# Kernel tuning notes

Measured on AMD Instinct MI355X. Metric: run time of the kernel, lower is better.

The kernel has to match this reference:

```python
import jax, jax.numpy as jnp
import numpy as np

NGRID, NLAYER = 8192, 24
NPERIODS, NOBS, NC = 50, 4096, 200
SIGMA = 1.0
VREF = 3.0          # reference crustal Vs (km/s) for depth-sensitivity scale
RAYLEIGH_FACTOR = 0.92


def setup_inputs() -> dict:
    key = jax.random.key(0)
    k1, k2, k3 = jax.random.split(key, 3)
    # S-wave velocity model, 2.0-4.0 km/s, flattened as in log_prob(Vs_flat)
    Vs_flat = (2.0 + 2.0 * jax.random.uniform(k1, (NGRID, NLAYER))).reshape(-1).astype(jnp.float32)
    # Ray-path averaging matrix: nonnegative, rows sum to 1 (slowness average)
    A = jax.random.uniform(k2, (NOBS, NGRID), dtype=jnp.float32)
    A = A / A.sum(axis=1, keepdims=True)
    # Beamforming energy spectra per observation pair: (Nobs, Nperiods, Nc)
    energy = jax.random.uniform(k3, (NOBS, NPERIODS, NC), dtype=jnp.float32)
    # Monotone phase-velocity axis per observation: (Nobs, Nc)
    c_axis = jnp.zeros((NOBS, NC), jnp.float32) + jnp.linspace(1.5, 5.0, NC, dtype=jnp.float32)
    thick = jnp.full((NLAYER,), 2.0, jnp.float32)          # 2 km layers
    periods = jnp.linspace(1.0, 60.0, NPERIODS, dtype=jnp.float32)
    return {"Vs_flat": Vs_flat, "A": A, "energy": energy, "c_axis": c_axis,
            "thick": thick, "periods": periods}


def _dispersion_all_cells(Vs, thick, periods):
    # Differentiable surrogate for the batched surf96 forward across all grid cells.
    # Vs: (G, L), thick: (L,), periods: (P,)  ->  c_true: (G, P)
    z = jnp.cumsum(thick) - 0.5 * thick                      # layer-center depths (L,)
    depth_scale = VREF * periods / 3.0                       # ~ sensing depth per period (P,)
    w = jnp.exp(-z[None, :] / depth_scale[:, None]) * thick[None, :]  # (P, L)
    w = w / w.sum(axis=1, keepdims=True)
    return RAYLEIGH_FACTOR * jnp.einsum('pl,gl->gp', w, Vs)  # (G, P)


def reference(Vs_flat, A, energy, c_axis, thick, periods):
    Vs = Vs_flat.reshape(NGRID, NLAYER)
    c_true = _dispersion_all_cells(Vs, thick, periods)       # (Ngrid, Nperiods)
    # _apply_A: slowness averaging along ray paths
    s_pred = A @ (1.0 / c_true)                              # (Nobs, Nperiods)
    c_pred = 1.0 / s_pred
    # _interp1d_torch, vectorized over all (obs, period) pairs
    idx = jax.vmap(jnp.searchsorted)(c_axis, c_pred)         # (Nobs, Nperiods)
    idx = jnp.clip(idx, 1, NC - 1)
    c0 = jnp.take_along_axis(c_axis, idx - 1, axis=1)
    c1 = jnp.take_along_axis(c_axis, idx, axis=1)
    e0 = jnp.take_along_axis(energy, (idx - 1)[:, :, None], axis=2)[..., 0]
    e1 = jnp.take_along_axis(energy, idx[:, :, None], axis=2)[..., 0]
    w = (c_pred - c0) / (c1 - c0 + 1e-12)
    e_interp = e0 + w * (e1 - e0)
    e_max = energy.max(axis=-1)                              # (Nobs, Nperiods)
    log_like = -jnp.sum(e_max - e_interp) / (SIGMA ** 2)
    return log_like
```

## Files before the change

### kernel.cpp

```cpp
#include <hip/hip_runtime.h>

#define NGRID 8192
#define NLAYER 24
#define NPERIODS 50
#define NOBS 4096
#define NC 200
#define PP 64
#define NSPLIT 16
#define GC (NGRID / NSPLIT)
#define KG 32
#define ASTR 36
#define NPW 13
#define NBINS 1024
#define OTILE 64
#define VREF 3.0f

__global__ __launch_bounds__(256) void k1_rpad(const float* __restrict__ Vs,
                                               const float* __restrict__ thick,
                                               const float* __restrict__ periods,
                                               float* __restrict__ r_pad,
                                               float* __restrict__ bins) {
    __shared__ float w_sh[NLAYER][NPERIODS];
    __shared__ float z_sh[NLAYER];
    int tid = threadIdx.x;
    if (blockIdx.x == 0) {
        for (int i = tid; i < NBINS; i += 256) bins[i] = 0.f;
    }
    if (tid < NLAYER) {
        float c = 0.f;
        for (int i = 0; i <= tid; ++i) c += thick[i];
        z_sh[tid] = c - 0.5f * thick[tid];
    }
    __syncthreads();
    if (tid < NPERIODS) {
        float ds = (VREF / 3.0f) * periods[tid];
        float tmp[NLAYER];
        float s = 0.f;
        #pragma unroll
        for (int l = 0; l < NLAYER; ++l) {
            float v = expf(-z_sh[l] / ds) * thick[l];
            tmp[l] = v; s += v;
        }
        float inv = 1.f / s;
        #pragma unroll
        for (int l = 0; l < NLAYER; ++l) w_sh[l][tid] = tmp[l] * inv;
    }
    __syncthreads();
    int idx = blockIdx.x * 256 + tid;
    int g = idx >> 6, p = idx & 63;
    float r = 0.f;
    if (p < NPERIODS) {
        const float4* vp = (const float4*)(Vs + (size_t)g * NLAYER);
        float s = 0.f;
        #pragma unroll
        for (int q = 0; q < NLAYER / 4; ++q) {
            float4 t = vp[q];
            s = fmaf(w_sh[4*q+0][p], t.x, s);
            s = fmaf(w_sh[4*q+1][p], t.y, s);
            s = fmaf(w_sh[4*q+2][p], t.z, s);
            s = fmaf(w_sh[4*q+3][p], t.w, s);
        }
        r = 1.0f / (0.92f * s);
    }
    r_pad[idx] = r;
}

__global__ __launch_bounds__(256) void k2_gemm(const float* __restrict__ A,
                                               const float* __restrict__ r_pad,
                                               float* __restrict__ partial_t) {
    __shared__ float Aw[OTILE * ASTR];
    int tid  = threadIdx.x;
    int lane = tid & 63;
    int wv   = __builtin_amdgcn_readfirstlane(tid >> 6);
    int o_base = blockIdx.x * OTILE;
    int split  = blockIdx.y;
    int pbase  = wv * NPW;

    float acc[NPW];
    #pragma unroll
    for (int p = 0; p < NPW; ++p) acc[p] = 0.f;

    int g_blk = split * GC;

    #pragma unroll 1
    for (int kt = 0; kt < GC / KG; ++kt) {
        int g0 = g_blk + kt * KG;
        __syncthreads();
        #pragma unroll
        for (int s = 0; s < 2; ++s) {
            int f   = s * 256 + tid;
            int row = f >> 3;
            int c4  = (f & 7) * 4;
            float4 t = *(const float4*)(A + (size_t)(o_base + row) * NGRID + g0 + c4);
            *(float4*)(Aw + row * ASTR + c4) = t;
        }
        __syncthreads();
        #pragma unroll 1
        for (int gg = 0; gg < KG; gg += 4) {
            float4 a4 = *(const float4*)(Aw + lane * ASTR + gg);
            const float* rr = r_pad + (size_t)(g0 + gg) * PP + pbase;
            #pragma unroll
            for (int j = 0; j < 4; ++j) {
                float aj = (j == 0) ? a4.x : (j == 1) ? a4.y : (j == 2) ? a4.z : a4.w;
                #pragma unroll
                for (int p = 0; p < NPW; ++p)
                    acc[p] = fmaf(aj, rr[j * PP + p], acc[p]);
            }
        }
    }

    float* outp = partial_t + (size_t)split * (NPERIODS * NOBS);
    #pragma unroll
    for (int p = 0; p < NPW; ++p) {
        int pp = pbase + p;
        if (pp < NPERIODS)
            outp[(size_t)pp * NOBS + o_base + lane] = acc[p];
    }
}

__global__ __launch_bounds__(256) void k2b_reduce(const float* __restrict__ partial_t,
                                                  float* __restrict__ cpred_t) {
    int idx = blockIdx.x * 256 + threadIdx.x;
    float s = 0.f;
    #pragma unroll
    for (int sp = 0; sp < NSPLIT; ++sp)
        s += partial_t[(size_t)sp * (NPERIODS * NOBS) + idx];
    cpred_t[idx] = 1.0f / s;
}

__global__ __launch_bounds__(256) void k3_main(const float* __restrict__ energy,
                                               const float* __restrict__ c_axis,
                                               const float* __restrict__ cpred_t,
                                               float* __restrict__ bins) {
    __shared__ float csh[NC];
    __shared__ float red[4];
    int tid  = threadIdx.x;
    int lane = tid & 63;
    int wv   = tid >> 6;
    int o    = blockIdx.x;

    if (tid < NC) csh[tid] = c_axis[(size_t)o * NC + tid];
    __syncthreads();

    bool act = lane < NC / 4;
    float4 ca = act ? *(const float4*)(csh + 4 * lane) : make_float4(9e30f, 9e30f, 9e30f, 9e30f);
    const float* ebase = energy + (size_t)o * NPERIODS * NC;
    float local = 0.f;

    for (int p0 = wv; p0 < NPERIODS; p0 += 8) {
        int p1 = p0 + 4;
        bool has1 = p1 < NPERIODS;
        int p1c = has1 ? p1 : p0;
        float cpA = cpred_t[(size_t)p0 * NOBS + o];
        float cpB = cpred_t[(size_t)p1c * NOBS + o];
        const float* erA = ebase + (size_t)p0 * NC;
        const float* erB = ebase + (size_t)p1c * NC;
        float4 eA = act ? *(const float4*)(erA + 4 * lane) : make_float4(-1e30f, -1e30f, -1e30f, -1e30f);
        float4 eB = act ? *(const float4*)(erB + 4 * lane) : make_float4(-1e30f, -1e30f, -1e30f, -1e30f);

        int cntA = __popcll(__ballot(ca.x < cpA)) + __popcll(__ballot(ca.y < cpA))
                 + __popcll(__ballot(ca.z < cpA)) + __popcll(__ballot(ca.w < cpA));
        int cntB = __popcll(__ballot(ca.x < cpB)) + __popcll(__ballot(ca.y < cpB))
                 + __popcll(__ballot(ca.z < cpB)) + __popcll(__ballot(ca.w < cpB));

        float mA = fmaxf(fmaxf(eA.x, eA.y), fmaxf(eA.z, eA.w));
        float mB = fmaxf(fmaxf(eB.x, eB.y), fmaxf(eB.z, eB.w));
        #pragma unroll
        for (int m = 32; m; m >>= 1) {
            mA = fmaxf(mA, __shfl_xor(mA, m, 64));
            mB = fmaxf(mB, __shfl_xor(mB, m, 64));
        }

        int iA = cntA < 1 ? 1 : (cntA > NC - 1 ? NC - 1 : cntA);
        int iB = cntB < 1 ? 1 : (cntB > NC - 1 ? NC - 1 : cntB);

        int a0 = iA - 1, a1 = iA, b0 = iB - 1, b1 = iB;
        float sA0 = ((a0 & 3) == 0) ? eA.x : ((a0 & 3) == 1) ? eA.y : ((a0 & 3) == 2) ? eA.z : eA.w;
        float sA1 = ((a1 & 3) == 0) ? eA.x : ((a1 & 3) == 1) ? eA.y : ((a1 & 3) == 2) ? eA.z : eA.w;
        float sB0 = ((b0 & 3) == 0) ? eB.x : ((b0 & 3) == 1) ? eB.y : ((b0 & 3) == 2) ? eB.z : eB.w;
        float sB1 = ((b1 & 3) == 0) ? eB.x : ((b1 & 3) == 1) ? eB.y : ((b1 & 3) == 2) ? eB.z : eB.w;
        float e0A = __shfl(sA0, a0 >> 2, 64), e1A = __shfl(sA1, a1 >> 2, 64);
        float e0B = __shfl(sB0, b0 >> 2, 64), e1B = __shfl(sB1, b1 >> 2, 64);

        float c0A = csh[a0], c1A = csh[a1];
        float c0B = csh[b0], c1B = csh[b1];
        float wA = (cpA - c0A) / (c1A - c0A + 1e-12f);
        float wB = (cpB - c0B) / (c1B - c0B + 1e-12f);
        float eiA = fmaf(wA, e1A - e0A, e0A);
        float eiB = fmaf(wB, e1B - e0B, e0B);
        local += mA - eiA;
        local += has1 ? (mB - eiB) : 0.f;
    }
    if (lane == 0) red[wv] = local;
    __syncthreads();
    if (tid == 0)
        atomicAdd(&bins[blockIdx.x & (NBINS - 1)], red[0] + red[1] + red[2] + red[3]);
}

__global__ __launch_bounds__(256) void k4_final(const float* __restrict__ bins,
                                                float* __restrict__ out) {
    __shared__ float red[4];
    int tid = threadIdx.x;
    float s = 0.f;
    for (int i = tid; i < NBINS; i += 256) s += bins[i];
    #pragma unroll
    for (int m = 32; m; m >>= 1) s += __shfl_xor(s, m, 64);
    int lane = tid & 63, wv = tid >> 6;
    if (lane == 0) red[wv] = s;
    __syncthreads();
    if (tid == 0) out[0] = -(red[0] + red[1] + red[2] + red[3]);
}

extern "C" void kernel_launch(void* const* d_in, const int* in_sizes, int n_in,
                              void* d_out, int out_size, void* d_ws, size_t ws_size,
                              hipStream_t stream) {
    const float* Vs      = (const float*)d_in[0];
    const float* A       = (const float*)d_in[1];
    const float* energy  = (const float*)d_in[2];
    const float* c_axis  = (const float*)d_in[3];
    const float* thick   = (const float*)d_in[4];
    const float* periods = (const float*)d_in[5];
    float* out = (float*)d_out;

    float* ws        = (float*)d_ws;
    float* r_pad     = ws;
    float* partial_t = r_pad + (size_t)NGRID * PP;
    float* cpred_t   = partial_t + (size_t)NSPLIT * NPERIODS * NOBS;
    float* bins      = cpred_t + (size_t)NPERIODS * NOBS;

    hipLaunchKernelGGL(k1_rpad, dim3((NGRID * 64) / 256), dim3(256), 0, stream,
                       Vs, thick, periods, r_pad, bins);
    hipLaunchKernelGGL(k2_gemm, dim3(NOBS / OTILE, NSPLIT), dim3(256), 0, stream,
                       A, r_pad, partial_t);
    hipLaunchKernelGGL(k2b_reduce, dim3((NPERIODS * NOBS) / 256), dim3(256), 0, stream,
                       partial_t, cpred_t);
    hipLaunchKernelGGL(k3_main, dim3(NOBS), dim3(256), 0, stream,
                       energy, c_axis, cpred_t, bins);
    hipLaunchKernelGGL(k4_final, dim3(1), dim3(256), 0, stream, bins, out);
}
```

Measured before the change: 391.2 us.

## Double-buffer A tiles in GEMM with 8 waves and stage energy in LDS

The GEMM kernel moves to 512 threads (8 waves, 7 periods each) and double-buffers the A tile in shared memory. The next tile's global load is issued before computing on the current one, and there is one barrier per iteration instead of two. The interpolation kernel now copies each observation's full energy block into padded shared memory and has lanes map to periods, with each wave scanning a quarter of the c axis for max and count. This replaces per-period ballots and shuffles. It raises LDS use to about 40KB per block in the interpolation kernel, which may limit occupancy.

```diff
diff --git a/kernel.cpp b/kernel.cpp
--- a/kernel.cpp
+++ b/kernel.cpp
@@ -9,8 +9,11 @@
 #define NSPLIT 16
 #define GC (NGRID / NSPLIT)
 #define KG 32
+#define NKT (GC / KG)
 #define ASTR 36
-#define NPW 13
+#define WPB 8
+#define NPW 7
+#define ESTR 201
 #define NBINS 1024
 #define OTILE 64
 #define VREF 3.0f
@@ -65,10 +68,10 @@
     r_pad[idx] = r;
 }
 
-__global__ __launch_bounds__(256) void k2_gemm(const float* __restrict__ A,
+__global__ __launch_bounds__(512) void k2_gemm(const float* __restrict__ A,
                                                const float* __restrict__ r_pad,
                                                float* __restrict__ partial_t) {
-    __shared__ float Aw[OTILE * ASTR];
+    __shared__ float Aw[2][OTILE * ASTR];
     int tid  = threadIdx.x;
     int lane = tid & 63;
     int wv   = __builtin_amdgcn_readfirstlane(tid >> 6);
@@ -81,23 +84,26 @@
     for (int p = 0; p < NPW; ++p) acc[p] = 0.f;
 
     int g_blk = split * GC;
+    int srow = tid >> 3;
+    int sc4  = (tid & 7) * 4;
+    const float* Abase = A + (size_t)(o_base + srow) * NGRID + sc4 + g_blk;
+
+    {
+        float4 t = *(const float4*)(Abase);
+        *(float4*)(&Aw[0][srow * ASTR + sc4]) = t;
+    }
 
     #pragma unroll 1
-    for (int kt = 0; kt < GC / KG; ++kt) {
+    for (int kt = 0; kt < NKT; ++kt) {
+        int cur = kt & 1;
+        __syncthreads();
+        int ktn = (kt + 1 < NKT) ? kt + 1 : NKT - 1;
+        float4 tnext = *(const float4*)(Abase + ktn * KG);
+
         int g0 = g_blk + kt * KG;
-        __syncthreads();
-        #pragma unroll
-        for (int s = 0; s < 2; ++s) {
-            int f   = s * 256 + tid;
-            int row = f >> 3;
-            int c4  = (f & 7) * 4;
-            float4 t = *(const float4*)(A + (size_t)(o_base + row) * NGRID + g0 + c4);
-            *(float4*)(Aw + row * ASTR + c4) = t;
-        }
-        __syncthreads();
         #pragma unroll 1
         for (int gg = 0; gg < KG; gg += 4) {
-            float4 a4 = *(const float4*)(Aw + lane * ASTR + gg);
+            float4 a4 = *(const float4*)(&Aw[cur][lane * ASTR + gg]);
             const float* rr = r_pad + (size_t)(g0 + gg) * PP + pbase;
             #pragma unroll
             for (int j = 0; j < 4; ++j) {
@@ -107,6 +113,7 @@
                     acc[p] = fmaf(aj, rr[j * PP + p], acc[p]);
             }
         }
+        *(float4*)(&Aw[cur ^ 1][srow * ASTR + sc4]) = tnext;
     }
 
     float* outp = partial_t + (size_t)split * (NPERIODS * NOBS);
@@ -132,69 +139,60 @@
                                                const float* __restrict__ c_axis,
                                                const float* __restrict__ cpred_t,
                                                float* __restrict__ bins) {
+    __shared__ float esh[NPERIODS * ESTR];
     __shared__ float csh[NC];
-    __shared__ float red[4];
+    __shared__ float cpsh[64];
+    __shared__ float cntp[4][64];
+    __shared__ float maxp[4][64];
     int tid  = threadIdx.x;
     int lane = tid & 63;
     int wv   = tid >> 6;
     int o    = blockIdx.x;
 
+    const float* eb = energy + (size_t)o * NPERIODS * NC;
+    for (int i = tid; i < (NPERIODS * NC) / 4; i += 256) {
+        int r_ = i / 50;
+        int c_ = (i - r_ * 50) * 4;
+        float4 v = *(const float4*)(eb + (size_t)i * 4);
+        float* d = esh + r_ * ESTR + c_;
+        d[0] = v.x; d[1] = v.y; d[2] = v.z; d[3] = v.w;
+    }
     if (tid < NC) csh[tid] = c_axis[(size_t)o * NC + tid];
-    __syncthreads();
-
-    bool act = lane < NC / 4;
-    float4 ca = act ? *(const float4*)(csh + 4 * lane) : make_float4(9e30f, 9e30f, 9e30f, 9e30f);
-    const float* ebase = energy + (size_t)o * NPERIODS * NC;
-    float local = 0.f;
-
-    for (int p0 = wv; p0 < NPERIODS; p0 += 8) {
-        int p1 = p0 + 4;
-        bool has1 = p1 < NPERIODS;
-        int p1c = has1 ? p1 : p0;
-        float cpA = cpred_t[(size_t)p0 * NOBS + o];
-        float cpB = cpred_t[(size_t)p1c * NOBS + o];
-        const float* erA = ebase + (size_t)p0 * NC;
-        const float* erB = ebase + (size_t)p1c * NC;
-        float4 eA = act ? *(const float4*)(erA + 4 * lane) : make_float4(-1e30f, -1e30f, -1e30f, -1e30f);
-        float4 eB = act ? *(const float4*)(erB + 4 * lane) : make_float4(-1e30f, -1e30f, -1e30f, -1e30f);
-
-        int cntA = __popcll(__ballot(ca.x < cpA)) + __popcll(__ballot(ca.y < cpA))
-                 + __popcll(__ballot(ca.z < cpA)) + __popcll(__ballot(ca.w < cpA));
-        int cntB = __popcll(__ballot(ca.x < cpB)) + __popcll(__ballot(ca.y < cpB))
-                 + __popcll(__ballot(ca.z < cpB)) + __popcll(__ballot(ca.w < cpB));
-
-        float mA = fmaxf(fmaxf(eA.x, eA.y), fmaxf(eA.z, eA.w));
-        float mB = fmaxf(fmaxf(eB.x, eB.y), fmaxf(eB.z, eB.w));
-        #pragma unroll
-        for (int m = 32; m; m >>= 1) {
-            mA = fmaxf(mA, __shfl_xor(mA, m, 64));
-            mB = fmaxf(mB, __shfl_xor(mB, m, 64));
-        }
-
-        int iA = cntA < 1 ? 1 : (cntA > NC - 1 ? NC - 1 : cntA);
-        int iB = cntB < 1 ? 1 : (cntB > NC - 1 ? NC - 1 : cntB);
-
-        int a0 = iA - 1, a1 = iA, b0 = iB - 1, b1 = iB;
-        float sA0 = ((a0 & 3) == 0) ? eA.x : ((a0 & 3) == 1) ? eA.y : ((a0 & 3) == 2) ? eA.z : eA.w;
-        float sA1 = ((a1 & 3) == 0) ? eA.x : ((a1 & 3) == 1) ? eA.y : ((a1 & 3) == 2) ? eA.z : eA.w;
-        float sB0 = ((b0 & 3) == 0) ? eB.x : ((b0 & 3) == 1) ? eB.y : ((b0 & 3) == 2) ? eB.z : eB.w;
-        float sB1 = ((b1 & 3) == 0) ? eB.x : ((b1 & 3) == 1) ? eB.y : ((b1 & 3) == 2) ? eB.z : eB.w;
-        float e0A = __shfl(sA0, a0 >> 2, 64), e1A = __shfl(sA1, a1 >> 2, 64);
-        float e0B = __shfl(sB0, b0 >> 2, 64), e1B = __shfl(sB1, b1 >> 2, 64);
-
-        float c0A = csh[a0], c1A = csh[a1];
-        float c0B = csh[b0], c1B = csh[b1];
-        float wA = (cpA - c0A) / (c1A - c0A + 1e-12f);
-        float wB = (cpB - c0B) / (c1B - c0B + 1e-12f);
-        float eiA = fmaf(wA, e1A - e0A, e0A);
-        float eiB = fmaf(wB, e1B - e0B, e0B);
-        local += mA - eiA;
-        local += has1 ? (mB - eiB) : 0.f;
-    }
-    if (lane == 0) red[wv] = local;
-    __syncthreads();
-    if (tid == 0)
-        atomicAdd(&bins[blockIdx.x & (NBINS - 1)], red[0] + red[1] + red[2] + red[3]);
+    if (tid < 64) cpsh[tid] = (tid < NPERIODS) ? cpred_t[(size_t)tid * NOBS + o] : 0.f;
+    __syncthreads();
+
+    int pr = lane < NPERIODS ? lane : 0;
+    float cp = cpsh[lane];
+    float mx = -1e30f, cnt = 0.f;
+    int cbase = wv * 50;
+    #pragma unroll 2
+    for (int c = 0; c < 50; ++c) {
+        float ev  = esh[pr * ESTR + cbase + c];
+        float cav = csh[cbase + c];
+        mx = fmaxf(mx, ev);
+        cnt += (cav < cp) ? 1.f : 0.f;
+    }
+    cntp[wv][lane] = cnt;
+    maxp[wv][lane] = mx;
+    __syncthreads();
+
+    float contrib = 0.f;
+    if (wv == 0) {
+        if (lane < NPERIODS) {
+            float ct = cntp[0][lane] + cntp[1][lane] + cntp[2][lane] + cntp[3][lane];
+            float m  = fmaxf(fmaxf(maxp[0][lane], maxp[1][lane]),
+                             fmaxf(maxp[2][lane], maxp[3][lane]));
+            int idx = (int)ct;
+            idx = idx < 1 ? 1 : (idx > NC - 1 ? NC - 1 : idx);
+            float c0 = csh[idx - 1], c1 = csh[idx];
+            float e0 = esh[lane * ESTR + idx - 1], e1 = esh[lane * ESTR + idx];
+            float w  = (cp - c0) / (c1 - c0 + 1e-12f);
+            contrib = m - fmaf(w, e1 - e0, e0);
+        }
+        #pragma unroll
+        for (int m2 = 32; m2; m2 >>= 1) contrib += __shfl_xor(contrib, m2, 64);
+        if (lane == 0) atomicAdd(&bins[o & (NBINS - 1)], contrib);
+    }
 }
 
 __global__ __launch_bounds__(256) void k4_final(const float* __restrict__ bins,
@@ -230,7 +228,7 @@
 
     hipLaunchKernelGGL(k1_rpad, dim3((NGRID * 64) / 256), dim3(256), 0, stream,
                        Vs, thick, periods, r_pad, bins);
-    hipLaunchKernelGGL(k2_gemm, dim3(NOBS / OTILE, NSPLIT), dim3(256), 0, stream,
+    hipLaunchKernelGGL(k2_gemm, dim3(NOBS / OTILE, NSPLIT), dim3(512), 0, stream,
                        A, r_pad, partial_t);
     hipLaunchKernelGGL(k2b_reduce, dim3((NPERIODS * NOBS) / 256), dim3(256), 0, stream,
                        partial_t, cpred_t);
```

After: 392.3 us. No clear change (+0.3%).
